# Performance work log

Hardware: AMD Instinct MI355X
Metric: run time of the kernel (lower is better)

Reference implementation:

```python
import jax, jax.numpy as jnp
import numpy as np

N_NODES = 50000
N_EDGES = 800000
N_GRAPHS = 512
NEG_SLOPE = 0.2  # PyG GATConv default LeakyReLU slope


def _gat_layer(x, src, dst, W, a_src, a_dst, b, n_nodes):
    """PyG-style GATConv (concat=True, self-loops already in src/dst)."""
    H, C = a_src.shape
    h = (x @ W).reshape(n_nodes, H, C)            # [N, H, C]
    e_s = (h * a_src).sum(-1)                     # [N, H]
    e_d = (h * a_dst).sum(-1)                     # [N, H]
    e = jax.nn.leaky_relu(e_s[src] + e_d[dst], NEG_SLOPE)  # [E, H]
    # segment softmax over destination nodes
    m = jax.ops.segment_max(e, dst, num_segments=n_nodes)
    w = jnp.exp(e - m[dst])
    s = jax.ops.segment_sum(w, dst, num_segments=n_nodes)
    alpha = w / (s[dst] + 1e-16)                  # [E, H]
    out = jax.ops.segment_sum(h[src] * alpha[:, :, None], dst, num_segments=n_nodes)
    return out.reshape(n_nodes, H * C) + b


def setup_inputs() -> dict:
    key = jax.random.key(0)
    ks = jax.random.split(key, 16)
    x = jax.random.normal(ks[0], (N_NODES, 2), dtype=jnp.float32)
    edge_index = jax.random.randint(ks[1], (2, N_EDGES), 0, N_NODES, dtype=jnp.int64 if jax.config.jax_enable_x64 else jnp.int32)
    batch = jnp.sort(jax.random.randint(ks[2], (N_NODES,), 0, N_GRAPHS))
    g = lambda k, shape: (jax.random.normal(k, shape, dtype=jnp.float32) * 0.1)
    return {
        "x": x, "edge_index": edge_index, "batch": batch,
        "W1": g(ks[3], (2, 64)),   "a1s": g(ks[4], (8, 8)),  "a1d": g(ks[5], (8, 8)),  "b1": jnp.zeros((64,), jnp.float32),
        "W2": g(ks[6], (64, 128)), "a2s": g(ks[7], (8, 16)), "a2d": g(ks[8], (8, 16)), "b2": jnp.zeros((128,), jnp.float32),
        "W3": g(ks[9], (128, 128)),"a3s": g(ks[10], (8, 16)),"a3d": g(ks[11], (8, 16)),"b3": jnp.zeros((128,), jnp.float32),
        "fc1W": g(ks[12], (128, 32)), "fc1b": jnp.zeros((32,), jnp.float32),
        "fc2W": g(ks[13], (32, 10)),  "fc2b": jnp.zeros((10,), jnp.float32),
    }


def reference(x, edge_index, batch, W1, a1s, a1d, b1, W2, a2s, a2d, b2, W3, a3s, a3d, b3, fc1W, fc1b, fc2W, fc2b):
    n = x.shape[0]
    loop = jnp.arange(n, dtype=edge_index.dtype)
    src = jnp.concatenate([edge_index[0], loop])  # add self-loops (PyG default)
    dst = jnp.concatenate([edge_index[1], loop])
    h = jax.nn.elu(_gat_layer(x, src, dst, W1, a1s, a1d, b1, n))
    h = jax.nn.elu(_gat_layer(h, src, dst, W2, a2s, a2d, b2, n))
    h = _gat_layer(h, src, dst, W3, a3s, a3d, b3, n)
    # global mean pool over graphs
    sums = jax.ops.segment_sum(h, batch, num_segments=N_GRAPHS)
    cnt = jax.ops.segment_sum(jnp.ones((n,), h.dtype), batch, num_segments=N_GRAPHS)
    pooled = sums / jnp.maximum(cnt, 1.0)[:, None]   # [G, 128]
    z = jax.nn.relu(pooled @ fc1W + fc1b)
    return jax.nn.log_softmax(z @ fc2W + fc2b, axis=1)
```

## Files before the change

### kernel.cpp

```cpp
#include <hip/hip_runtime.h>
#include <cstddef>
#include <cstdint>

typedef __attribute__((ext_vector_type(8))) short bf16x8;
typedef __attribute__((ext_vector_type(4))) float floatx4;
typedef __attribute__((ext_vector_type(2))) float v2f;


__device__ __forceinline__ unsigned bf16pair(float a, float b) {
    unsigned ua = __float_as_uint(a), ub = __float_as_uint(b);
    ua += 0x7fffu + ((ua >> 16) & 1u);
    ub += 0x7fffu + ((ub >> 16) & 1u);
    return (ua >> 16) | (ub & 0xffff0000u);
}
__device__ __forceinline__ unsigned short bf16one(float a) {
    unsigned ua = __float_as_uint(a);
    ua += 0x7fffu + ((ua >> 16) & 1u);
    return (unsigned short)(ua >> 16);
}

#define BSTRIDE 8192


__global__ __launch_bounds__(256) void prep_k(
    const int* __restrict__ edge, unsigned* __restrict__ barr,
    int* __restrict__ bcnt, int E, int EA, int B1,
    const float* __restrict__ W2, unsigned short* __restrict__ Wt2,
    const float* __restrict__ W3, unsigned short* __restrict__ Wt3,
    const float* __restrict__ x, const float* __restrict__ W1,
    const float* __restrict__ a1s, const float* __restrict__ a1d,
    unsigned char* __restrict__ h8a, float* __restrict__ es,
    float* __restrict__ ed, int N) {
    int tid = threadIdx.x;
    if ((int)blockIdx.x < B1) {
        __shared__ int h[256];
        __shared__ int lbase[256];
        h[tid] = 0;
        __syncthreads();
        int start = blockIdx.x * 4096;
        unsigned ent[16];
        int lp[16];
#pragma unroll
        for (int k = 0; k < 16; ++k) {
            int i = start + k * 256 + tid;
            if (i < EA) {
                int s, d;
                if (i < E) { s = edge[i]; d = edge[E + i]; }
                else { s = i - E; d = s; }
                int b = d >> 8;
                ent[k] = (unsigned)s | ((unsigned)(d & 255) << 16) | ((unsigned)b << 24);
                lp[k] = atomicAdd(&h[b], 1);
            } else {
                ent[k] = 0xffffffffu;
                lp[k] = 0;
            }
        }
        __syncthreads();
        lbase[tid] = h[tid] ? atomicAdd(&bcnt[tid], h[tid]) : 0;
        __syncthreads();
#pragma unroll
        for (int k = 0; k < 16; ++k) {
            if (ent[k] != 0xffffffffu) {
                int b = ent[k] >> 24;
                int pos = lbase[b] + lp[k];
                if (pos < BSTRIDE)
                    barr[(size_t)b * BSTRIDE + pos] = ent[k] & 0x00ffffffu;
            }
        }
        return;
    }
    if ((int)blockIdx.x < B1 + 96) {
        int rel = blockIdx.x - B1;
        const float* W = (rel < 32) ? W2 : W3;
        unsigned short* Wt = (rel < 32) ? Wt2 : Wt3;
        int total = (rel < 32) ? 8192 : 16384;
        int o = ((rel < 32) ? rel : rel - 32) * 256 + tid;
        if (o < total) {
            int j = o & 7, lane = (o >> 3) & 63, ct = (o >> 9) & 7, ks = o >> 12;
            int k = ks * 32 + (lane >> 4) * 8 + j;
            int n = ct * 16 + (lane & 15);
            Wt[o] = bf16one(W[k * 128 + n]);
        }
        return;
    }
    int wave = tid >> 6, lane = tid & 63;
    int nbase = (blockIdx.x - B1 - 96) * 32;
    float w0 = W1[lane], w1 = W1[64 + lane];
    float as = a1s[lane], ad = a1d[lane];
    int head = lane >> 3;
#pragma unroll
    for (int it = 0; it < 8; ++it) {
        int n = nbase + it * 4 + wave;
        int nc = (n < N) ? n : N - 1;
        float2 xv = ((const float2*)x)[nc];
        float h = xv.x * w0 + xv.y * w1;
        float ps = h * as, pd = h * ad;
#pragma unroll
        for (int off = 1; off < 8; off <<= 1) {
            ps += __shfl_xor(ps, off);
            pd += __shfl_xor(pd, off);
        }
        if (n < N) {
            unsigned d = __builtin_amdgcn_cvt_pk_fp8_f32(h, h, 0, false);
            h8a[(size_t)n * 64 + lane] = (unsigned char)d;
            if ((lane & 7) == 0) { es[n * 8 + head] = ps; ed[n * 8 + head] = pd; }
        }
    }
}


__global__ __launch_bounds__(256) void bucket2_k(const unsigned* __restrict__ barr,
                                                 const int* __restrict__ bcnt,
                                                 int* __restrict__ offsets,
                                                 int* __restrict__ esrc,
                                                 int N, int EA, int nbuck) {
    __shared__ int sd[256];
    __shared__ int bb[256];
    __shared__ int cur[256];
    int b = blockIdx.x, tid = threadIdx.x;
    int v = (tid < nbuck) ? bcnt[tid] : 0;
    sd[tid] = v;
    __syncthreads();
    for (int off = 1; off < 256; off <<= 1) {
        int t = (tid >= off) ? sd[tid - off] : 0;
        __syncthreads();
        sd[tid] += t;
        __syncthreads();
    }
    bb[tid] = sd[tid] - v;
    __syncthreads();
    int bbase = bb[b];
    if (b == 0 && tid == 0) offsets[N] = EA;

    int cnt = bcnt[b];
    const unsigned* arr = barr + (size_t)b * BSTRIDE;
    sd[tid] = 0;
    __syncthreads();
    for (int i = tid; i < cnt; i += 256)
        atomicAdd(&sd[(arr[i] >> 16) & 0xff], 1);
    __syncthreads();
    v = sd[tid];
    for (int off = 1; off < 256; off <<= 1) {
        int t = (tid >= off) ? sd[tid - off] : 0;
        __syncthreads();
        sd[tid] += t;
        __syncthreads();
    }
    int base = bbase + sd[tid] - v;
    int n = b * 256 + tid;
    if (n < N) offsets[n] = base;
    cur[tid] = base;
    __syncthreads();
    for (int i = tid; i < cnt; i += 256) {
        unsigned e = arr[i];
        int pos = atomicAdd(&cur[(e >> 16) & 0xff], 1);
        esrc[pos] = (int)(e & 0xffffu);
    }
}


template <int IN>
__global__ __launch_bounds__(256) void gemm_mfma_k(
    const unsigned short* __restrict__ a16, const unsigned short* __restrict__ Wt,
    const float* __restrict__ a_s, const float* __restrict__ a_d,
    unsigned char* __restrict__ h8, float* __restrict__ es, float* __restrict__ ed,
    int n_nodes) {
    constexpr int KSTEPS = IN / 32;
    __shared__ float Cl[64 * 132];
    int wave = threadIdx.x >> 6, lane = threadIdx.x & 63;
    int q = lane >> 4, m = lane & 15;
    int rbase = blockIdx.x * 64;

    floatx4 acc[8];
#pragma unroll
    for (int ct = 0; ct < 8; ++ct) acc[ct] = (floatx4){0.f, 0.f, 0.f, 0.f};

    int ra = rbase + wave * 16 + m;
    if (ra >= n_nodes) ra = n_nodes - 1;
    const unsigned short* arow = a16 + (size_t)ra * IN + q * 8;

#pragma unroll
    for (int ks = 0; ks < KSTEPS; ++ks) {
        bf16x8 af = *(const bf16x8*)(arow + ks * 32);
        const unsigned short* wp = Wt + ((size_t)(ks * 8) * 64 + lane) * 8;
#pragma unroll
        for (int ct = 0; ct < 8; ++ct) {
            bf16x8 bf = *(const bf16x8*)(wp + (size_t)ct * 64 * 8);
            acc[ct] = __builtin_amdgcn_mfma_f32_16x16x32_bf16(af, bf, acc[ct], 0, 0, 0);
        }
    }

#pragma unroll
    for (int ct = 0; ct < 8; ++ct)
#pragma unroll
        for (int i = 0; i < 4; ++i)
            Cl[(wave * 16 + q * 4 + i) * 132 + ct * 16 + m] = acc[ct][i];
    __syncthreads();

    int rl = threadIdx.x >> 2, part = threadIdx.x & 3;
    int r = rbase + rl;
    if (r < n_nodes) {
        const float* cp = &Cl[rl * 132 + part * 32];
        float e0s = 0.f, e0d = 0.f, e1s = 0.f, e1d = 0.f;
#pragma unroll
        for (int c = 0; c < 16; ++c) {
            float v = cp[c];
            int ai = part * 32 + c;
            e0s += v * a_s[ai];
            e0d += v * a_d[ai];
        }
#pragma unroll
        for (int c = 16; c < 32; ++c) {
            float v = cp[c];
            int ai = part * 32 + c;
            e1s += v * a_s[ai];
            e1d += v * a_d[ai];
        }
        unsigned pk8[8];
#pragma unroll
        for (int u = 0; u < 8; ++u) {
            unsigned d = __builtin_amdgcn_cvt_pk_fp8_f32(cp[4 * u], cp[4 * u + 1], 0, false);
            d = __builtin_amdgcn_cvt_pk_fp8_f32(cp[4 * u + 2], cp[4 * u + 3], d, true);
            pk8[u] = d;
        }
        uint4* hp = (uint4*)(h8 + (size_t)r * 128) + part * 2;
        hp[0] = make_uint4(pk8[0], pk8[1], pk8[2], pk8[3]);
        hp[1] = make_uint4(pk8[4], pk8[5], pk8[6], pk8[7]);
        es[r * 8 + 2 * part] = e0s;
        es[r * 8 + 2 * part + 1] = e1s;
        ed[r * 8 + 2 * part] = e0d;
        ed[r * 8 + 2 * part + 1] = e1d;
    }
}


template <int NCOL, bool ELU>
__global__ __launch_bounds__(256) void gat_k(
    const void* __restrict__ hsrc, const float* __restrict__ es,
    const float* __restrict__ ed, const int* __restrict__ offsets,
    const int* __restrict__ esrc, const float* __restrict__ bias,
    void* __restrict__ outp, int n_nodes) {
    constexpr int UPL = NCOL / 32;
    int wave = threadIdx.x >> 6, lane = threadIdx.x & 63;
    int n = blockIdx.x * 4 + wave;
    if (n >= n_nodes) return;
    int g = lane >> 4;
    int l = lane & 15;
    int head = l >> 1;
    float edn = ed[n * 8 + head];
    int start = offsets[n], end = offsets[n + 1];

    v2f acc2[UPL];
#pragma unroll
    for (int k = 0; k < UPL; ++k) acc2[k] = (v2f){0.f, 0.f};
    float s = 0.f;

#pragma unroll 2
    for (int j = start; j < end; j += 4) {
        int jj = j + g;
        bool act = (jj < end);
        int src = esrc[act ? jj : end - 1];
        float e0 = es[(size_t)src * 8 + head] + edn;
        float e = fmaxf(e0, 0.2f * e0);
        float p = act ? __expf(e) : 0.f;
        s += p;
        v2f p2 = (v2f){p, p};
        if constexpr (UPL == 4) {
            uint2 u = *(const uint2*)((const unsigned char*)hsrc +
                                      (size_t)src * 128 + 8 * l);
            acc2[0] += p2 * (v2f)__builtin_amdgcn_cvt_pk_f32_fp8(u.x, false);
            acc2[1] += p2 * (v2f)__builtin_amdgcn_cvt_pk_f32_fp8(u.x, true);
            acc2[2] += p2 * (v2f)__builtin_amdgcn_cvt_pk_f32_fp8(u.y, false);
            acc2[3] += p2 * (v2f)__builtin_amdgcn_cvt_pk_f32_fp8(u.y, true);
        } else {
            unsigned u = *(const unsigned*)((const unsigned char*)hsrc +
                                            (size_t)src * 64 + 4 * l);
            acc2[0] += p2 * (v2f)__builtin_amdgcn_cvt_pk_f32_fp8(u, false);
            acc2[1] += p2 * (v2f)__builtin_amdgcn_cvt_pk_f32_fp8(u, true);
        }
    }

    float v[2 * UPL];
#pragma unroll
    for (int k = 0; k < UPL; ++k) { v[2 * k] = acc2[k].x; v[2 * k + 1] = acc2[k].y; }

    s += __shfl_xor(s, 16);
    s += __shfl_xor(s, 32);
#pragma unroll
    for (int k = 0; k < 2 * UPL; ++k) {
        v[k] += __shfl_xor(v[k], 16);
        v[k] += __shfl_xor(v[k], 32);
    }

    if (g == 0) {
        float r = 1.f / (s + 1e-16f);
#pragma unroll
        for (int k = 0; k < 2 * UPL; ++k) {
            float b = bias[(2 * UPL) * l + k];
            float t = v[k] * r + b;
            if constexpr (ELU) t = (t > 0.f) ? t : expm1f(t);
            v[k] = t;
        }
        if constexpr (UPL == 4) {
            uint4 pk;
            pk.x = bf16pair(v[0], v[1]);
            pk.y = bf16pair(v[2], v[3]);
            pk.z = bf16pair(v[4], v[5]);
            pk.w = bf16pair(v[6], v[7]);
            ((uint4*)outp)[(size_t)n * 16 + l] = pk;
        } else {
            uint2 pk;
            pk.x = bf16pair(v[0], v[1]);
            pk.y = bf16pair(v[2], v[3]);
            ((uint2*)outp)[(size_t)n * 16 + l] = pk;
        }
    }
}


__global__ __launch_bounds__(64) void pool_k(const unsigned* __restrict__ hu,
                                             const int* __restrict__ batch,
                                             float* __restrict__ sums,
                                             float* __restrict__ cnt, int n_nodes) {
    int c = threadIdx.x;
    int base = blockIdx.x * 32;
    float a0 = 0.f, a1 = 0.f, cacc = 0.f;
    int gprev = -1;
    for (int k = 0; k < 32; k++) {
        int n = base + k;
        if (n >= n_nodes) break;
        int g = batch[n];
        if (g != gprev) {
            if (gprev >= 0) {
                atomicAdd(&sums[gprev * 128 + 2 * c], a0);
                atomicAdd(&sums[gprev * 128 + 2 * c + 1], a1);
                if (c == 0) atomicAdd(&cnt[gprev], cacc);
            }
            a0 = 0.f; a1 = 0.f; cacc = 0.f; gprev = g;
        }
        unsigned u = hu[(size_t)n * 64 + c];
        a0 += __uint_as_float(u << 16);
        a1 += __uint_as_float(u & 0xffff0000u);
        cacc += 1.f;
    }
    if (gprev >= 0) {
        atomicAdd(&sums[gprev * 128 + 2 * c], a0);
        atomicAdd(&sums[gprev * 128 + 2 * c + 1], a1);
        if (c == 0) atomicAdd(&cnt[gprev], cacc);
    }
}


__global__ __launch_bounds__(64) void fc_k(const float* __restrict__ sums,
                                           const float* __restrict__ cnt,
                                           const float* __restrict__ fc1W,
                                           const float* __restrict__ fc1b,
                                           const float* __restrict__ fc2W,
                                           const float* __restrict__ fc2b,
                                           float* __restrict__ out) {
    int g = blockIdx.x, lane = threadIdx.x;
    __shared__ float p[128];
    __shared__ float z[32];
    __shared__ float logits[10];
    float inv = 1.f / fmaxf(cnt[g], 1.f);
    p[lane] = sums[g * 128 + lane] * inv;
    p[lane + 64] = sums[g * 128 + 64 + lane] * inv;
    __syncthreads();
    if (lane < 32) {
        float a = fc1b[lane];
        for (int k = 0; k < 128; k++) a += p[k] * fc1W[k * 32 + lane];
        z[lane] = fmaxf(a, 0.f);
    }
    __syncthreads();
    if (lane < 10) {
        float a = fc2b[lane];
        for (int k = 0; k < 32; k++) a += z[k] * fc2W[k * 10 + lane];
        logits[lane] = a;
    }
    __syncthreads();
    if (lane < 10) {
        float mx = logits[0];
#pragma unroll
        for (int i = 1; i < 10; i++) mx = fmaxf(mx, logits[i]);
        float se = 0.f;
#pragma unroll
        for (int i = 0; i < 10; i++) se += __expf(logits[i] - mx);
        out[g * 10 + lane] = logits[lane] - mx - logf(se);
    }
}


extern "C" void kernel_launch(void* const* d_in, const int* in_sizes, int n_in,
                              void* d_out, int out_size, void* d_ws, size_t ws_size,
                              hipStream_t stream) {
    const float* x = (const float*)d_in[0];
    const int* edge = (const int*)d_in[1];
    const int* batch = (const int*)d_in[2];
    const float* W1 = (const float*)d_in[3];
    const float* a1s = (const float*)d_in[4];
    const float* a1d = (const float*)d_in[5];
    const float* b1 = (const float*)d_in[6];
    const float* W2 = (const float*)d_in[7];
    const float* a2s = (const float*)d_in[8];
    const float* a2d = (const float*)d_in[9];
    const float* b2 = (const float*)d_in[10];
    const float* W3 = (const float*)d_in[11];
    const float* a3s = (const float*)d_in[12];
    const float* a3d = (const float*)d_in[13];
    const float* b3 = (const float*)d_in[14];
    const float* fc1W = (const float*)d_in[15];
    const float* fc1b = (const float*)d_in[16];
    const float* fc2W = (const float*)d_in[17];
    const float* fc2b = (const float*)d_in[18];
    float* out = (float*)d_out;

    const int N = in_sizes[0] / 2;
    const int E = in_sizes[1] / 2;
    const int EA = E + N;
    const int NG = out_size / 10;
    const int NBUCK = (N + 255) >> 8;
    const int B1 = (EA + 4095) / 4096;
    const int G1 = (N + 31) / 32;

    char* p = (char*)d_ws;
    unsigned* h3b16 = (unsigned*)p; p += (size_t)N * 64 * 4;
    unsigned char* h8 = (unsigned char*)p; p += (size_t)N * 128;
    unsigned char* h8a = (unsigned char*)p; p += (size_t)N * 64;
    unsigned short* a16a = (unsigned short*)p; p += (size_t)N * 64 * 2;
    unsigned short* a16b = (unsigned short*)p; p += (size_t)N * 128 * 2;
    unsigned short* Wt2 = (unsigned short*)p; p += (size_t)64 * 128 * 2;
    unsigned short* Wt3 = (unsigned short*)p; p += (size_t)128 * 128 * 2;
    float* es = (float*)p;  p += (size_t)N * 8 * 4;
    float* ed = (float*)p;  p += (size_t)N * 8 * 4;
    float* sums = (float*)p; p += (size_t)NG * 128 * 4;
    float* cnt = (float*)p;  p += (size_t)NG * 4;
    int* bcnt = (int*)p;     p += 256 * 4;
    int* offsets = (int*)p;  p += (size_t)(N + 1) * 4;
    int* esrc = (int*)p;     p += (size_t)(EA + 8) * 4;
    unsigned* barr = (unsigned*)p; p += (size_t)NBUCK * BSTRIDE * 4;

    hipMemsetAsync(sums, 0, ((size_t)NG * 128 + NG + 256) * 4, stream);

    prep_k<<<B1 + 96 + G1, 256, 0, stream>>>(
        edge, barr, bcnt, E, EA, B1, W2, Wt2, W3, Wt3,
        x, W1, a1s, a1d, h8a, es, ed, N);
    bucket2_k<<<NBUCK, 256, 0, stream>>>(barr, bcnt, offsets, esrc, N, EA, NBUCK);

    int mblocks = (N + 63) / 64;
    int ablocks = (N + 3) / 4;
    gat_k<64, true><<<ablocks, 256, 0, stream>>>(h8a, es, ed, offsets, esrc, b1, a16a, N);
    gemm_mfma_k<64><<<mblocks, 256, 0, stream>>>(a16a, Wt2, a2s, a2d, h8, es, ed, N);
    gat_k<128, true><<<ablocks, 256, 0, stream>>>(h8, es, ed, offsets, esrc, b2, a16b, N);
    gemm_mfma_k<128><<<mblocks, 256, 0, stream>>>(a16b, Wt3, a3s, a3d, h8, es, ed, N);
    gat_k<128, false><<<ablocks, 256, 0, stream>>>(h8, es, ed, offsets, esrc, b3, h3b16, N);

    pool_k<<<(N + 31) / 32, 64, 0, stream>>>(h3b16, batch, sums, cnt, N);
    fc_k<<<NG, 64, 0, stream>>>(sums, cnt, fc1W, fc1b, fc2W, fc2b, out);
}
```

Baseline: 282.6 us.

## Process two nodes per wavefront in GAT aggregation with wider per-lane loads

The GAT aggregation kernel now assigns two destination nodes per 64-lane wavefront instead of one, with 8 lanes per edge slot each handling a whole head (16 or 8 fp8 values via a single wide load). The esrc array gets 8 zero-padded tail entries so the edge-index load no longer needs clamping. This raises per-lane work and memory-access width and halves the block count, aiming to cut idle lanes on low-degree nodes and per-wave overhead. It doubles accumulator registers, which could reduce occupancy, and drops the unroll pragma.

```diff
diff --git a/kernel.cpp b/kernel.cpp
--- a/kernel.cpp
+++ b/kernel.cpp
@@ -131,6 +131,7 @@
     __syncthreads();
     int bbase = bb[b];
     if (b == 0 && tid == 0) offsets[N] = EA;
+    if (b == 0 && tid < 8) esrc[EA + tid] = 0;
 
     int cnt = bcnt[b];
     const unsigned* arr = barr + (size_t)b * BSTRIDE;
@@ -236,63 +237,68 @@
 
 template <int NCOL, bool ELU>
 __global__ __launch_bounds__(256) void gat_k(
-    const void* __restrict__ hsrc, const float* __restrict__ es,
+    const unsigned char* __restrict__ hsrc, const float* __restrict__ es,
     const float* __restrict__ ed, const int* __restrict__ offsets,
     const int* __restrict__ esrc, const float* __restrict__ bias,
     void* __restrict__ outp, int n_nodes) {
-    constexpr int UPL = NCOL / 32;
+    constexpr int UPL = NCOL / 16;
     int wave = threadIdx.x >> 6, lane = threadIdx.x & 63;
-    int n = blockIdx.x * 4 + wave;
-    if (n >= n_nodes) return;
-    int g = lane >> 4;
-    int l = lane & 15;
-    int head = l >> 1;
-    float edn = ed[n * 8 + head];
-    int start = offsets[n], end = offsets[n + 1];
+    int half = lane >> 5;
+    int hl = lane & 31;
+    int slot = hl >> 3;
+    int l = lane & 7;
+    int n = blockIdx.x * 8 + wave * 2 + half;
+    bool valid = (n < n_nodes);
+    int nc = valid ? n : 0;
+    float edn = ed[nc * 8 + l];
+    int start = valid ? offsets[nc] : 0;
+    int end = valid ? offsets[nc + 1] : 0;
 
     v2f acc2[UPL];
 #pragma unroll
     for (int k = 0; k < UPL; ++k) acc2[k] = (v2f){0.f, 0.f};
     float s = 0.f;
 
-#pragma unroll 2
     for (int j = start; j < end; j += 4) {
-        int jj = j + g;
+        int jj = j + slot;
         bool act = (jj < end);
-        int src = esrc[act ? jj : end - 1];
-        float e0 = es[(size_t)src * 8 + head] + edn;
+        int src = esrc[jj];
+        float e0 = es[(size_t)src * 8 + l] + edn;
         float e = fmaxf(e0, 0.2f * e0);
         float p = act ? __expf(e) : 0.f;
         s += p;
         v2f p2 = (v2f){p, p};
-        if constexpr (UPL == 4) {
-            uint2 u = *(const uint2*)((const unsigned char*)hsrc +
-                                      (size_t)src * 128 + 8 * l);
+        if constexpr (NCOL == 128) {
+            uint4 u = *(const uint4*)(hsrc + (size_t)src * 128 + 16 * l);
             acc2[0] += p2 * (v2f)__builtin_amdgcn_cvt_pk_f32_fp8(u.x, false);
             acc2[1] += p2 * (v2f)__builtin_amdgcn_cvt_pk_f32_fp8(u.x, true);
             acc2[2] += p2 * (v2f)__builtin_amdgcn_cvt_pk_f32_fp8(u.y, false);
             acc2[3] += p2 * (v2f)__builtin_amdgcn_cvt_pk_f32_fp8(u.y, true);
+            acc2[4] += p2 * (v2f)__builtin_amdgcn_cvt_pk_f32_fp8(u.z, false);
+            acc2[5] += p2 * (v2f)__builtin_amdgcn_cvt_pk_f32_fp8(u.z, true);
+            acc2[6] += p2 * (v2f)__builtin_amdgcn_cvt_pk_f32_fp8(u.w, false);
+            acc2[7] += p2 * (v2f)__builtin_amdgcn_cvt_pk_f32_fp8(u.w, true);
         } else {
-            unsigned u = *(const unsigned*)((const unsigned char*)hsrc +
-                                            (size_t)src * 64 + 4 * l);
-            acc2[0] += p2 * (v2f)__builtin_amdgcn_cvt_pk_f32_fp8(u, false);
-            acc2[1] += p2 * (v2f)__builtin_amdgcn_cvt_pk_f32_fp8(u, true);
-        }
-    }
-
+            uint2 u = *(const uint2*)(hsrc + (size_t)src * 64 + 8 * l);
+            acc2[0] += p2 * (v2f)__builtin_amdgcn_cvt_pk_f32_fp8(u.x, false);
+            acc2[1] += p2 * (v2f)__builtin_amdgcn_cvt_pk_f32_fp8(u.x, true);
+            acc2[2] += p2 * (v2f)__builtin_amdgcn_cvt_pk_f32_fp8(u.y, false);
+            acc2[3] += p2 * (v2f)__builtin_amdgcn_cvt_pk_f32_fp8(u.y, true);
+        }
+    }
+
+    s += __shfl_xor(s, 8);
+    s += __shfl_xor(s, 16);
     float v[2 * UPL];
 #pragma unroll
     for (int k = 0; k < UPL; ++k) { v[2 * k] = acc2[k].x; v[2 * k + 1] = acc2[k].y; }
-
-    s += __shfl_xor(s, 16);
-    s += __shfl_xor(s, 32);
 #pragma unroll
     for (int k = 0; k < 2 * UPL; ++k) {
+        v[k] += __shfl_xor(v[k], 8);
         v[k] += __shfl_xor(v[k], 16);
-        v[k] += __shfl_xor(v[k], 32);
-    }
-
-    if (g == 0) {
+    }
+
+    if (slot == 0 && valid) {
         float r = 1.f / (s + 1e-16f);
 #pragma unroll
         for (int k = 0; k < 2 * UPL; ++k) {
@@ -301,18 +307,16 @@
             if constexpr (ELU) t = (t > 0.f) ? t : expm1f(t);
             v[k] = t;
         }
-        if constexpr (UPL == 4) {
-            uint4 pk;
-            pk.x = bf16pair(v[0], v[1]);
-            pk.y = bf16pair(v[2], v[3]);
-            pk.z = bf16pair(v[4], v[5]);
-            pk.w = bf16pair(v[6], v[7]);
-            ((uint4*)outp)[(size_t)n * 16 + l] = pk;
+        if constexpr (NCOL == 128) {
+            uint4* op = (uint4*)outp + (size_t)n * 16 + 2 * l;
+            op[0] = make_uint4(bf16pair(v[0], v[1]), bf16pair(v[2], v[3]),
+                               bf16pair(v[4], v[5]), bf16pair(v[6], v[7]));
+            op[1] = make_uint4(bf16pair(v[8], v[9]), bf16pair(v[10], v[11]),
+                               bf16pair(v[12], v[13]), bf16pair(v[14], v[15]));
         } else {
-            uint2 pk;
-            pk.x = bf16pair(v[0], v[1]);
-            pk.y = bf16pair(v[2], v[3]);
-            ((uint2*)outp)[(size_t)n * 16 + l] = pk;
+            ((uint4*)outp)[(size_t)n * 8 + l] =
+                make_uint4(bf16pair(v[0], v[1]), bf16pair(v[2], v[3]),
+                           bf16pair(v[4], v[5]), bf16pair(v[6], v[7]));
         }
     }
 }
@@ -447,7 +451,7 @@
     bucket2_k<<<NBUCK, 256, 0, stream>>>(barr, bcnt, offsets, esrc, N, EA, NBUCK);
 
     int mblocks = (N + 63) / 64;
-    int ablocks = (N + 3) / 4;
+    int ablocks = (N + 7) / 8;
     gat_k<64, true><<<ablocks, 256, 0, stream>>>(h8a, es, ed, offsets, esrc, b1, a16a, N);
     gemm_mfma_k<64><<<mblocks, 256, 0, stream>>>(a16a, Wt2, a2s, a2d, h8, es, ed, N);
     gat_k<128, true><<<ablocks, 256, 0, stream>>>(h8, es, ed, offsets, esrc, b2, a16b, N);
```

Measured after the change: 278.3 us. About the same (-1.5%).
